# Kernel optimization log

Hardware: AMD Instinct MI355X
Metric: run time of the kernel (lower is better)

## Reference

```python
import jax, jax.numpy as jnp
import numpy as np

LEAF = 32
DEPTH = 12
N = LEAF * 2 ** DEPTH  # 131072 nodes
MAX_RANK = 64
RANK_SCALE = 2.0
BATCH = 32


def _rank_schedule():
    # N^(2/3) rank scaling, coarse (level 0) -> fine, matching the torch code
    ranks = []
    for level in range(DEPTH):
        block_size = LEAF * 2 ** (DEPTH - 1 - level)
        r = max(4, min(MAX_RANK, int(round(RANK_SCALE * block_size ** (2.0 / 3.0)))))
        if r % 2 != 0:
            r = min(MAX_RANK, r + 1)
        ranks.append(r)
    return ranks


RANKS = _rank_schedule()  # [64]*9 + [52, 32, 20]


def setup_inputs() -> dict:
    key = jax.random.key(0)
    keys = jax.random.split(key, DEPTH + 2)
    num_blocks = N // LEAF
    eye = jnp.broadcast_to(jnp.eye(LEAF, dtype=jnp.float32), (1, num_blocks, LEAF, LEAF))
    leaf_blocks = eye + 0.01 * jax.random.normal(keys[0], (1, num_blocks, LEAF, LEAF), jnp.float32)
    inp = {
        'x': jax.random.normal(keys[1], (BATCH, N), jnp.float32),
        'leaf_blocks': leaf_blocks,
        'hodlr_scale': jnp.asarray(1.0, jnp.float32),
    }
    for i, r in enumerate(RANKS):
        inp[f'u{i}'] = 0.05 * jax.random.normal(keys[2 + i], (1, N, r), jnp.float32)
    return inp


def _apply_hodlr(leaf_blocks, hodlr_scale, us, x):
    B = x.shape[0]
    num_blocks = N // LEAF
    # Dense block-diagonal leaf multiply: y_k = A_k x_k for each 32x32 block
    xb = x.reshape(B, num_blocks, LEAF)
    y = jnp.einsum('kts,nks->nkt', leaf_blocks[0], xb).reshape(B, N)
    s2 = hodlr_scale * hodlr_scale  # factors are (u*s, u*s)
    for level, u in enumerate(us):
        bsz = LEAF * 2 ** (DEPTH - 1 - level)  # block size at this level
        p = N // (2 * bsz)                      # number of sibling pairs
        r = u.shape[-1]
        Ur = u[0].reshape(p, 2, bsz, r)
        xr = x.reshape(B, p, 2, bsz)
        # project each block: t[n,p,c,:] = U[p,c]^T x[n,p,c]
        t = jnp.einsum('pcsr,npcs->npcr', Ur, xr)
        # off-diagonal coupling: each block receives its sibling's projection
        t = t[:, :, ::-1, :]
        y = y + s2 * jnp.einsum('pcsr,npcr->npcs', Ur, t).reshape(B, N)
    return y


def reference(x, leaf_blocks, hodlr_scale, u0, u1, u2, u3, u4, u5, u6, u7, u8, u9, u10, u11):
    us = [u0, u1, u2, u3, u4, u5, u6, u7, u8, u9, u10, u11]
    return _apply_hodlr(leaf_blocks, hodlr_scale, us, x)
```

## Files before the change

### kernel.cpp

```cpp
#include <hip/hip_runtime.h>

#define NN 131072
#define BB 32

struct LevelParams {
  const float* u[12];
  int t_off[12];
  int r[12];
  int rpad[12];
  int lb[12];
};

__global__ __launch_bounds__(256, 3)
void tpass_kernel(const float* __restrict__ x, float* __restrict__ t,
                  float* __restrict__ part, LevelParams P) {
  __shared__ float xT[128 * 36];
  __shared__ float Ut[128 * 64];

  const int bid = blockIdx.x;
  const int l = bid >> 7;
  const int chunk = bid & 127;
  const int tid = threadIdx.x;

  const float* __restrict__ u = P.u[l];
  const int r = P.r[l];
  const int rpad = P.rpad[l];
  const int lb = P.lb[l];
  float* __restrict__ tl = t + P.t_off[l];

  const int G = rpad >> 3;
  const int split = tid >> 5;
  const int lane32 = tid & 31;
  const int n0 = (lane32 >> 3) << 3;
  const int jg = lane32 & 7;
  const int j0 = jg << 3;
  const bool active = (jg < G);

  const int lg = (lb >= 7) ? 3 : (lb - 4);
  const int gsz = 1 << lg;

  float acc[8][8];
  #pragma unroll
  for (int a = 0; a < 8; a++)
    #pragma unroll
    for (int b = 0; b < 8; b++) acc[a][b] = 0.f;

  const int Rc = chunk << 10;
  const int r4 = rpad >> 2;
  const int uslots = 32 * rpad;

  for (int sub = 0; sub < 8; sub++) {
    const int s0 = Rc + (sub << 7);
    #pragma unroll
    for (int rep = 0; rep < 16; rep++) {
      int idx = rep * 256 + tid;
      int ss = idx & 127;
      int n = idx >> 7;
      xT[ss * 36 + n] = x[n * NN + s0 + ss];
    }
    for (int slot = tid; slot < uslots; slot += 256) {
      int row = slot / r4;
      int c4 = slot - row * r4;
      int j = c4 << 2;
      float4 v;
      if (j < r) v = *(const float4*)&u[(s0 + row) * r + j];
      else       v = make_float4(0.f, 0.f, 0.f, 0.f);
      *(float4*)&Ut[row * rpad + j] = v;
    }
    __syncthreads();

    if (active) {
      const int sl0 = split << 4;
      #pragma unroll 4
      for (int ss = 0; ss < 16; ss++) {
        const int sl = sl0 + ss;
        float4 xa = *(const float4*)&xT[sl * 36 + n0];
        float4 xb = *(const float4*)&xT[sl * 36 + n0 + 4];
        float4 ua = *(const float4*)&Ut[sl * rpad + j0];
        float4 ub = *(const float4*)&Ut[sl * rpad + j0 + 4];
        float xs[8] = {xa.x, xa.y, xa.z, xa.w, xb.x, xb.y, xb.z, xb.w};
        float us[8] = {ua.x, ua.y, ua.z, ua.w, ub.x, ub.y, ub.z, ub.w};
        #pragma unroll
        for (int a = 0; a < 8; a++)
          #pragma unroll
          for (int b = 0; b < 8; b++)
            acc[a][b] += xs[a] * us[b];
      }
    }

    const bool fl = (sub == 7) || (((s0 + 128) >> lb) != (s0 >> lb));
    if (fl) {
      __syncthreads();
      for (int h = gsz >> 1; h >= 1; h >>= 1) {
        const int sig = split & (gsz - 1);
        if (active && sig >= h && sig < (h << 1)) {
          int rid = split - h;
          int slot = (rid >> lg) * h + (rid & (gsz - 1));
          float* dst = Ut + slot * 2048 + lane32;
          #pragma unroll
          for (int a = 0; a < 8; a++)
            #pragma unroll
            for (int b = 0; b < 8; b++)
              dst[(a * 8 + b) * 32] = acc[a][b];
        }
        __syncthreads();
        if (active && (split & (gsz - 1)) < h) {
          int slot = (split >> lg) * h + (split & (gsz - 1));
          const float* src = Ut + slot * 2048 + lane32;
          #pragma unroll
          for (int a = 0; a < 8; a++)
            #pragma unroll
            for (int b = 0; b < 8; b++)
              acc[a][b] += src[(a * 8 + b) * 32];
        }
        __syncthreads();
      }
      if (active && (split & (gsz - 1)) == 0) {
        const int grow = s0 + (split << 4);
        const int gseg = grow >> lb;
        float* outp = (lb >= 10) ? (part + (l * 128 + chunk) * 2048)
                                 : (tl + gseg * 32 * rpad);
        float* base = outp + n0 * rpad + j0;
        #pragma unroll
        for (int a = 0; a < 8; a++) {
          *(float4*)&base[a * rpad]     = make_float4(acc[a][0], acc[a][1], acc[a][2], acc[a][3]);
          *(float4*)&base[a * rpad + 4] = make_float4(acc[a][4], acc[a][5], acc[a][6], acc[a][7]);
        }
      }
      #pragma unroll
      for (int a = 0; a < 8; a++)
        #pragma unroll
        for (int b = 0; b < 8; b++) acc[a][b] = 0.f;
    }
    __syncthreads();
  }
}

__global__ __launch_bounds__(256)
void reduce_kernel(const float* __restrict__ part, float* __restrict__ t,
                   LevelParams P) {
  int b = blockIdx.x;
  int l = 0, segs = 2;
  while (b >= segs) { b -= segs; l++; segs <<= 1; }
  const int nch = 64 >> l;
  const int tid = threadIdx.x;
  const float* src = part + (size_t)(l * 128 + b * nch) * 2048 + tid * 8;
  float s0 = 0.f, s1 = 0.f, s2 = 0.f, s3 = 0.f, s4 = 0.f, s5 = 0.f, s6 = 0.f, s7 = 0.f;
  for (int k = 0; k < nch; k++) {
    float4 v0 = *(const float4*)&src[k * 2048];
    float4 v1 = *(const float4*)&src[k * 2048 + 4];
    s0 += v0.x; s1 += v0.y; s2 += v0.z; s3 += v0.w;
    s4 += v1.x; s5 += v1.y; s6 += v1.z; s7 += v1.w;
  }
  float* dst = t + P.t_off[l] + b * 2048 + tid * 8;
  *(float4*)dst = make_float4(s0, s1, s2, s3);
  *(float4*)&dst[4] = make_float4(s4, s5, s6, s7);
}

__global__ __launch_bounds__(256, 2)
void ypass_kernel(const float* __restrict__ x,
                  const float* __restrict__ leaf,
                  const float* __restrict__ scale,
                  const float* __restrict__ t,
                  float* __restrict__ out,
                  LevelParams P) {
  __shared__ float smem[17664];

  const int bid = blockIdx.x;
  const int tid = threadIdx.x;
  const int R0 = bid << 8;
  const int ig = tid >> 3;
  const int ng = tid & 7;
  const int i0l = ig << 3;
  const int n0 = ng << 2;

  const float sc = scale[0];
  const float s2 = sc * sc;

  float acc[8][4];
  #pragma unroll
  for (int k = 0; k < 8; k++)
    #pragma unroll
    for (int m = 0; m < 4; m++) acc[k][m] = 0.f;

  {
    float* xT = smem;
    float* Lb = smem + 9216;
    #pragma unroll 4
    for (int rep = 0; rep < 32; rep++) {
      xT[tid * 36 + rep] = x[rep * NN + R0 + tid];
    }
    const float* lbase = leaf + (R0 >> 5) * 1024;
    for (int slot = tid; slot < 2048; slot += 256) {
      int flat = slot << 2;
      float4 v = *(const float4*)&lbase[flat];
      int b = flat >> 10;
      int tt_ = (flat >> 5) & 31;
      int s = flat & 31;
      float* dst = &Lb[b * 1056 + tt_ * 33 + s];
      dst[0] = v.x; dst[1] = v.y; dst[2] = v.z; dst[3] = v.w;
    }
    __syncthreads();
    const int bl = ig >> 2;
    const int irow0 = (ig & 3) << 3;
    #pragma unroll 4
    for (int s = 0; s < 32; s++) {
      float4 xv = *(const float4*)&xT[(bl * 32 + s) * 36 + n0];
      float xs[4] = {xv.x, xv.y, xv.z, xv.w};
      #pragma unroll
      for (int k = 0; k < 8; k++) {
        float L = Lb[bl * 1056 + (irow0 + k) * 33 + s];
        #pragma unroll
        for (int m = 0; m < 4; m++) acc[k][m] += L * xs[m];
      }
    }
    __syncthreads();
  }

  float* ttl = smem;
  float* Uc  = smem + 6144;
  for (int l = 0; l < 12; l++) {
    const float* __restrict__ u = P.u[l];
    const int r = P.r[l], rpad = P.rpad[l], lb = P.lb[l];
    const float* tl = t + P.t_off[l];
    const int segfloats = 32 * rpad;
    const int span_sh = (lb >= 8) ? 0 : (8 - lb);
    const int total4 = (segfloats << span_sh) >> 2;
    const int bseg = R0 >> lb;
    for (int idx4 = tid; idx4 < total4; idx4 += 256) {
      int flat = idx4 << 2;
      int k = flat / segfloats;
      int rem = flat - k * segfloats;
      int sib = (bseg + k) ^ 1;
      float4 v = *(const float4*)&tl[sib * segfloats + rem];
      v.x *= s2; v.y *= s2; v.z *= s2; v.w *= s2;
      *(float4*)&ttl[flat] = v;
    }
    __syncthreads();
    const int kseg = i0l >> lb;
    const float* ttb = ttl + kseg * segfloats + n0 * rpad;
    const int nj = rpad >> 3;
    for (int jc = 0; jc < nj; jc++) {
      #pragma unroll
      for (int rep = 0; rep < 2; rep++) {
        int slot = rep * 256 + tid;
        int row = slot >> 1;
        int h = (slot & 1) << 2;
        int j = (jc << 3) + h;
        float4 v;
        if (j < r) v = *(const float4*)&u[(R0 + row) * r + j];
        else       v = make_float4(0.f, 0.f, 0.f, 0.f);
        *(float4*)&Uc[(row << 3) + h] = v;
      }
      __syncthreads();
      #pragma unroll
      for (int half = 0; half < 2; half++) {
        const int jb = (jc << 3) + (half << 2);
        float4 tv0 = *(const float4*)&ttb[0 * rpad + jb];
        float4 tv1 = *(const float4*)&ttb[1 * rpad + jb];
        float4 tv2 = *(const float4*)&ttb[2 * rpad + jb];
        float4 tv3 = *(const float4*)&ttb[3 * rpad + jb];
        #pragma unroll
        for (int k = 0; k < 8; k++) {
          float4 uv = *(const float4*)&Uc[((i0l + k) << 3) + (half << 2)];
          acc[k][0] += uv.x * tv0.x + uv.y * tv0.y + uv.z * tv0.z + uv.w * tv0.w;
          acc[k][1] += uv.x * tv1.x + uv.y * tv1.y + uv.z * tv1.z + uv.w * tv1.w;
          acc[k][2] += uv.x * tv2.x + uv.y * tv2.y + uv.z * tv2.z + uv.w * tv2.w;
          acc[k][3] += uv.x * tv3.x + uv.y * tv3.y + uv.z * tv3.z + uv.w * tv3.w;
        }
      }
      __syncthreads();
    }
  }

  #pragma unroll
  for (int m = 0; m < 4; m++) {
    float4 o0 = make_float4(acc[0][m], acc[1][m], acc[2][m], acc[3][m]);
    float4 o1 = make_float4(acc[4][m], acc[5][m], acc[6][m], acc[7][m]);
    float* dst = out + (n0 + m) * NN + R0 + i0l;
    *(float4*)&dst[0] = o0;
    *(float4*)&dst[4] = o1;
  }
}

extern "C" void kernel_launch(void* const* d_in, const int* in_sizes, int n_in,
                              void* d_out, int out_size, void* d_ws, size_t ws_size,
                              hipStream_t stream) {
  const float* x     = (const float*)d_in[0];
  const float* leaf  = (const float*)d_in[1];
  const float* scale = (const float*)d_in[2];

  static const int RANKS[12] = {64,64,64,64,64,64,64,64,64,52,32,20};
  LevelParams P;
  int off = 0;
  for (int l = 0; l < 12; l++) {
    P.u[l] = (const float*)d_in[3 + l];
    P.r[l] = RANKS[l];
    P.rpad[l] = (RANKS[l] + 7) & ~7;
    P.lb[l] = 16 - l;
    P.t_off[l] = off;
    off += (2 << l) * 32 * P.rpad[l];
  }

  float* t = (float*)d_ws;
  float* part = t + off;

  tpass_kernel<<<dim3(12 * 128), dim3(256), 0, stream>>>(x, t, part, P);
  reduce_kernel<<<dim3(254), dim3(256), 0, stream>>>(part, t, P);
  ypass_kernel<<<dim3(NN / 256), dim3(256), 0, stream>>>(x, leaf, scale, t,
                                                         (float*)d_out, P);
}
```

Baseline: 674.1 us.

## Read U factors directly from global in ypass, swizzle t tile, raise occupancy

The ypass kernel no longer stages U columns through shared memory in 8-column chunks with two barriers per chunk. Each thread now reads its 8 U rows straight from global memory inside a rank-templated inner loop. The sibling projection tile is stored with an XOR swizzle and a rank padding rounded to 32, and the leaf-block staging is split into two halves to shrink shared memory. Launch bounds go to 3 blocks per CU. This trades barrier and LDS traffic for uncoalesced per-thread global loads of U, which rely on cache hits, and adds register pressure from the templated unrolled loops.

```diff
diff --git a/kernel.cpp b/kernel.cpp
--- a/kernel.cpp
+++ b/kernel.cpp
@@ -157,14 +157,37 @@
   *(float4*)&dst[4] = make_float4(s4, s5, s6, s7);
 }
 
-__global__ __launch_bounds__(256, 2)
+template<int RC>
+__device__ __forceinline__ void level_mm(const float* __restrict__ ub,
+                                         const float* __restrict__ tt,
+                                         int ng, float acc[8][4]) {
+  constexpr int RPL = (RC + 31) & ~31;
+  #pragma unroll 4
+  for (int c4 = 0; c4 < (RC >> 2); c4++) {
+    const int tcol = ((c4 ^ ng) << 2);
+    float4 tv0 = *(const float4*)&tt[0 * RPL + tcol];
+    float4 tv1 = *(const float4*)&tt[1 * RPL + tcol];
+    float4 tv2 = *(const float4*)&tt[2 * RPL + tcol];
+    float4 tv3 = *(const float4*)&tt[3 * RPL + tcol];
+    #pragma unroll
+    for (int k = 0; k < 8; k++) {
+      float4 uv = *(const float4*)&ub[k * RC + (c4 << 2)];
+      acc[k][0] += uv.x * tv0.x + uv.y * tv0.y + uv.z * tv0.z + uv.w * tv0.w;
+      acc[k][1] += uv.x * tv1.x + uv.y * tv1.y + uv.z * tv1.z + uv.w * tv1.w;
+      acc[k][2] += uv.x * tv2.x + uv.y * tv2.y + uv.z * tv2.z + uv.w * tv2.w;
+      acc[k][3] += uv.x * tv3.x + uv.y * tv3.y + uv.z * tv3.z + uv.w * tv3.w;
+    }
+  }
+}
+
+__global__ __launch_bounds__(256, 3)
 void ypass_kernel(const float* __restrict__ x,
                   const float* __restrict__ leaf,
                   const float* __restrict__ scale,
                   const float* __restrict__ t,
                   float* __restrict__ out,
                   LevelParams P) {
-  __shared__ float smem[17664];
+  __shared__ float smem[13440];
 
   const int bid = blockIdx.x;
   const int tid = threadIdx.x;
@@ -190,87 +213,71 @@
     for (int rep = 0; rep < 32; rep++) {
       xT[tid * 36 + rep] = x[rep * NN + R0 + tid];
     }
-    const float* lbase = leaf + (R0 >> 5) * 1024;
-    for (int slot = tid; slot < 2048; slot += 256) {
-      int flat = slot << 2;
-      float4 v = *(const float4*)&lbase[flat];
-      int b = flat >> 10;
-      int tt_ = (flat >> 5) & 31;
-      int s = flat & 31;
-      float* dst = &Lb[b * 1056 + tt_ * 33 + s];
-      dst[0] = v.x; dst[1] = v.y; dst[2] = v.z; dst[3] = v.w;
-    }
-    __syncthreads();
     const int bl = ig >> 2;
     const int irow0 = (ig & 3) << 3;
-    #pragma unroll 4
-    for (int s = 0; s < 32; s++) {
-      float4 xv = *(const float4*)&xT[(bl * 32 + s) * 36 + n0];
-      float xs[4] = {xv.x, xv.y, xv.z, xv.w};
-      #pragma unroll
-      for (int k = 0; k < 8; k++) {
-        float L = Lb[bl * 1056 + (irow0 + k) * 33 + s];
-        #pragma unroll
-        for (int m = 0; m < 4; m++) acc[k][m] += L * xs[m];
+    for (int ch = 0; ch < 2; ch++) {
+      __syncthreads();
+      const float* lbase = leaf + ((R0 >> 5) + ch * 4) * 1024;
+      for (int slot = tid; slot < 1024; slot += 256) {
+        int flat = slot << 2;
+        float4 v = *(const float4*)&lbase[flat];
+        int b = flat >> 10;
+        int tt_ = (flat >> 5) & 31;
+        int s = flat & 31;
+        float* dst = &Lb[b * 1056 + tt_ * 33 + s];
+        dst[0] = v.x; dst[1] = v.y; dst[2] = v.z; dst[3] = v.w;
+      }
+      __syncthreads();
+      if ((bl >> 2) == ch) {
+        const int bll = bl & 3;
+        #pragma unroll 4
+        for (int s = 0; s < 32; s++) {
+          float4 xv = *(const float4*)&xT[((bl << 5) + s) * 36 + n0];
+          float xs[4] = {xv.x, xv.y, xv.z, xv.w};
+          #pragma unroll
+          for (int k = 0; k < 8; k++) {
+            float L = Lb[bll * 1056 + (irow0 + k) * 33 + s];
+            #pragma unroll
+            for (int m = 0; m < 4; m++) acc[k][m] += L * xs[m];
+          }
+        }
       }
     }
     __syncthreads();
   }
 
   float* ttl = smem;
-  float* Uc  = smem + 6144;
   for (int l = 0; l < 12; l++) {
     const float* __restrict__ u = P.u[l];
     const int r = P.r[l], rpad = P.rpad[l], lb = P.lb[l];
+    const int rpadL = (r + 31) & ~31;
     const float* tl = t + P.t_off[l];
-    const int segfloats = 32 * rpad;
+    const int segf_g = rpad << 5;
+    const int segf_l = rpadL << 5;
     const int span_sh = (lb >= 8) ? 0 : (8 - lb);
-    const int total4 = (segfloats << span_sh) >> 2;
     const int bseg = R0 >> lb;
+    const int total4 = (segf_g << span_sh) >> 2;
     for (int idx4 = tid; idx4 < total4; idx4 += 256) {
       int flat = idx4 << 2;
-      int k = flat / segfloats;
-      int rem = flat - k * segfloats;
+      int k, rem, n, c;
+      if (rpad == 64)      { k = flat >> 11; rem = flat & 2047; n = rem >> 6; c = rem & 63; }
+      else if (rpad == 32) { k = flat >> 10; rem = flat & 1023; n = rem >> 5; c = rem & 31; }
+      else { k = flat / segf_g; rem = flat - k * segf_g; n = rem / rpad; c = rem - n * rpad; }
       int sib = (bseg + k) ^ 1;
-      float4 v = *(const float4*)&tl[sib * segfloats + rem];
+      float4 v = *(const float4*)&tl[(size_t)sib * segf_g + rem];
       v.x *= s2; v.y *= s2; v.z *= s2; v.w *= s2;
-      *(float4*)&ttl[flat] = v;
+      int c4s = (((c >> 2) ^ ((n >> 2) & 7)) << 2);
+      *(float4*)&ttl[((k << 5) | n) * rpadL + c4s] = v;
     }
     __syncthreads();
     const int kseg = i0l >> lb;
-    const float* ttb = ttl + kseg * segfloats + n0 * rpad;
-    const int nj = rpad >> 3;
-    for (int jc = 0; jc < nj; jc++) {
-      #pragma unroll
-      for (int rep = 0; rep < 2; rep++) {
-        int slot = rep * 256 + tid;
-        int row = slot >> 1;
-        int h = (slot & 1) << 2;
-        int j = (jc << 3) + h;
-        float4 v;
-        if (j < r) v = *(const float4*)&u[(R0 + row) * r + j];
-        else       v = make_float4(0.f, 0.f, 0.f, 0.f);
-        *(float4*)&Uc[(row << 3) + h] = v;
-      }
-      __syncthreads();
-      #pragma unroll
-      for (int half = 0; half < 2; half++) {
-        const int jb = (jc << 3) + (half << 2);
-        float4 tv0 = *(const float4*)&ttb[0 * rpad + jb];
-        float4 tv1 = *(const float4*)&ttb[1 * rpad + jb];
-        float4 tv2 = *(const float4*)&ttb[2 * rpad + jb];
-        float4 tv3 = *(const float4*)&ttb[3 * rpad + jb];
-        #pragma unroll
-        for (int k = 0; k < 8; k++) {
-          float4 uv = *(const float4*)&Uc[((i0l + k) << 3) + (half << 2)];
-          acc[k][0] += uv.x * tv0.x + uv.y * tv0.y + uv.z * tv0.z + uv.w * tv0.w;
-          acc[k][1] += uv.x * tv1.x + uv.y * tv1.y + uv.z * tv1.z + uv.w * tv1.w;
-          acc[k][2] += uv.x * tv2.x + uv.y * tv2.y + uv.z * tv2.z + uv.w * tv2.w;
-          acc[k][3] += uv.x * tv3.x + uv.y * tv3.y + uv.z * tv3.z + uv.w * tv3.w;
-        }
-      }
-      __syncthreads();
-    }
+    const float* tt = ttl + kseg * segf_l + n0 * rpadL;
+    const float* ub = u + (size_t)(R0 + i0l) * r;
+    if (r == 64)      level_mm<64>(ub, tt, ng, acc);
+    else if (r == 52) level_mm<52>(ub, tt, ng, acc);
+    else if (r == 32) level_mm<32>(ub, tt, ng, acc);
+    else              level_mm<20>(ub, tt, ng, acc);
+    __syncthreads();
   }
 
   #pragma unroll
```

After: 745.6 us. 1.11x slower.
